# Kernel tuning notes

Hardware: AMD Instinct MI355X
Metric: run time of the kernel (lower is better)

Reference implementation:

```python
import jax, jax.numpy as jnp
import numpy as np

N, T0, T1 = 2, 4, 8
H, W = 128, 128
PD, AD = 4, 4
Z_POS, Z_APP = PD * PD, AD * AD
Z = Z_POS + Z_APP
KS, STRIDE, ROUTINGS = 3, 1, 3


def psquash(p, axis):
    return p / jnp.max(jnp.abs(p), axis=axis, keepdims=True)


def matwo_squash(p, axis):
    sq = jnp.sum(p * p, axis=axis, keepdims=True)
    return sq / (1.0 + sq) * p / jnp.sqrt(sq + 1e-9)


def setup_inputs() -> dict:
    key = jax.random.key(0)
    ks = jax.random.split(key, 5)
    return {
        "x": jax.random.normal(ks[0], (N, T0, Z, H, W), jnp.float32),
        "W_conv": jax.random.normal(ks[1], (T0, KS, KS, 1, T1), jnp.float32) * 0.1,
        "W_pos": jax.random.normal(ks[2], (T0, Z_POS, T1), jnp.float32) * 0.1,
        "W_app": jax.random.normal(ks[3], (T0, Z_APP, T1), jnp.float32) * 0.1,
        "b_app": jax.random.normal(ks[4], (T0, T1), jnp.float32) * 0.1,
    }


def _forward(x, W_conv, W_pos, W_app, b_app):
    n, t0, z0, h, w = x.shape
    t1 = W_conv.shape[-1]
    # per-input-capsule 2D conv: channels folded into batch, 1 -> t1 channels
    xt = x.transpose(1, 0, 2, 3, 4).reshape(t0, n * z0, h, w, 1)
    conv = jax.vmap(lambda u, k: jax.lax.conv_general_dilated(
        u, k, (STRIDE, STRIDE), 'SAME',
        dimension_numbers=('NHWC', 'HWIO', 'NHWC')))(xt, W_conv)
    h1, w1 = conv.shape[2], conv.shape[3]
    # [t0, N, z0, H1, W1, t1] -> [t0, N, H1, W1, t1, z0] -> flatten (t1,z0)
    u = conv.reshape(t0, n, z0, h1, w1, t1).transpose(0, 1, 3, 4, 5, 2)
    flat = u.reshape(t0, n, h1, w1, t1 * z0)
    # faithful replication of the original tf.split on the flattened (t1*z0) axis
    u_pos = flat[..., :t1 * Z_POS].reshape(t0, n, h1, w1, t1, PD, PD)
    u_app = flat[..., t1 * Z_POS:].reshape(t0, n, h1, w1, t1, AD, AD)

    # pose transform matrices: l2-normalize columns (axis=-2), coordinate addition
    mult_pos = W_pos.reshape(t0, t1, PD, PD)
    mult_pos = mult_pos / jnp.sqrt(
        jnp.maximum(jnp.sum(mult_pos * mult_pos, axis=-2, keepdims=True), 1e-12))
    coord = jnp.zeros((h1, w1, 1, PD, PD), x.dtype)
    coord = coord.at[:, :, 0, -1, 0].add(jnp.arange(w1, dtype=x.dtype)[None, :] / w1)
    coord = coord.at[:, :, 0, -1, 1].add(jnp.arange(h1, dtype=x.dtype)[:, None] / h1)
    mult_pos_hw = mult_pos[:, None, None] + coord[None]  # [t0,h1,w1,t1,PD,PD]
    u_hat_pos = jnp.einsum('cnhwtij,chwtjk->cnhwtik', u_pos, mult_pos_hw)

    mult_app = W_app.reshape(t0, t1, AD, AD)
    u_app = u_app + b_app[:, None, None, None, :, None, None]
    u_hat_app = jnp.einsum('cnhwtij,ctjk->cnhwtik', u_app, mult_app)

    u_hat = jnp.concatenate(
        [u_hat_pos.reshape(t0, n, h1, w1, t1, Z_POS),
         u_hat_app.reshape(t0, n, h1, w1, t1, Z_APP)], axis=-1)
    u_hat = u_hat.transpose(1, 5, 2, 3, 0, 4)  # [N, z1, H1, W1, t0, t1]

    # dual routing (sigmoid coupling, separate pos/app agreement)
    uh_pos, uh_app = u_hat[:, :Z_POS], u_hat[:, Z_POS:]
    b = jnp.zeros((n, h1, w1, t0, t1), x.dtype)
    for _ in range(ROUTINGS - 1):
        r = jax.nn.sigmoid(b)
        p = jnp.einsum('nzhwct,nhwct->nzhwt', u_hat, r)
        v_pos = psquash(p[:, :Z_POS], axis=1)
        v_app = matwo_squash(p[:, Z_POS:], axis=1)
        rout = (jnp.einsum('nzhwct,nzhwt->nhwct', uh_pos, v_pos)
                * jnp.einsum('nzhwct,nzhwt->nhwct', uh_app, v_app))
        b = b + rout
    c = jax.nn.sigmoid(b)
    p = jnp.einsum('nzhwct,nhwct->nzhwt', u_hat, c)
    v = jnp.concatenate([psquash(p[:, :Z_POS], axis=1),
                         matwo_squash(p[:, Z_POS:], axis=1)], axis=1)
    return v.transpose(0, 4, 1, 2, 3)  # [N, t1, z1, H1, W1]


def reference(x, W_conv, W_pos, W_app, b_app):
    return _forward(x, W_conv, W_pos, W_app, b_app)
```

## Files before the change

kernel.cpp:

```cpp
#include <hip/hip_runtime.h>
#include <cmath>


#define TH 2
#define TW 8
#define XR (TH + 2)
#define XC (TW + 2)
#define ZPAD 36

__device__ __forceinline__ float qsum4(float v) {
    int a = __builtin_amdgcn_mov_dpp(__float_as_int(v), 0xB1, 0xF, 0xF, true);
    v += __int_as_float(a);
    int b = __builtin_amdgcn_mov_dpp(__float_as_int(v), 0x4E, 0xF, 0xF, true);
    v += __int_as_float(b);
    return v;
}

__global__ __launch_bounds__(256)
__attribute__((amdgpu_waves_per_eu(4, 4)))
void caps_fused(const float* __restrict__ x,
                const float* __restrict__ Wc,
                const float* __restrict__ Wp,
                const float* __restrict__ Wa,
                const float* __restrict__ ba,
                float* __restrict__ out)
{
    __shared__ float xs[XR][XC][4][ZPAD];

    const int tid = threadIdx.x;
    const int n  = blockIdx.z;
    const int h0 = blockIdx.y * TH;
    const int w0 = blockIdx.x * TW;

    for (int e = tid; e < 128 * XR * XC; e += 256) {
        int col = e % XC;
        int tmp = e / XC;
        int row = tmp % XR;
        int cz  = tmp / XR;
        int gh = h0 - 1 + row;
        int gw = w0 - 1 + col;
        float v = 0.0f;
        if ((unsigned)gh < 128u && (unsigned)gw < 128u)
            v = x[(((size_t)(n * 128 + cz)) << 14) + (gh << 7) + gw];
        int z = cz & 31;
        int s = (row * XC + col) & 7;
        xs[row][col][cz >> 5][(((z >> 2) ^ s) << 2) | (z & 3)] = v;
    }

    const int p    = tid >> 5;
    const int lane = tid & 31;
    const int c    = lane & 3;
    const int t    = lane >> 2;
    const int chp  = t >> 1;
    const int q0   = (t & 1) << 2;

    float wp9[9], wa9[9];
#pragma unroll
    for (int i = 0; i < 9; ++i) {
        wp9[i] = Wc[(c * 9 + i) * 8 + chp];
        wa9[i] = Wc[(c * 9 + i) * 8 + 4 + chp];
    }
    float Mp[16], Ma[16];
#pragma unroll
    for (int q = 0; q < 16; ++q) {
        Mp[q] = Wp[c * 128 + t * 16 + q];
        Ma[q] = Wa[c * 128 + t * 16 + q];
    }
#pragma unroll
    for (int k = 0; k < 4; ++k) {
        float s = Mp[k] * Mp[k] + Mp[4 + k] * Mp[4 + k]
                + Mp[8 + k] * Mp[8 + k] + Mp[12 + k] * Mp[12 + k];
        float inv = __builtin_amdgcn_rsqf(fmaxf(s, 1e-12f));
        Mp[k] *= inv; Mp[4 + k] *= inv; Mp[8 + k] *= inv; Mp[12 + k] *= inv;
    }
    const float bap = ba[c * 8 + t];
    const float wx  = (float)(w0 + p) * (1.0f / 128.0f);

    __syncthreads();

    for (int g = 0; g < TH; ++g) {
        float up[16], ua[16];
#pragma unroll
        for (int q = 0; q < 16; ++q) { up[q] = 0.0f; ua[q] = 0.0f; }
#pragma unroll
        for (int dy = 0; dy < 3; ++dy) {
#pragma unroll
            for (int dx = 0; dx < 3; ++dx) {
                const int rr = g + dy, cc = p + dx;
                const int s = (rr * XC + cc) & 7;
                const float* bp = &xs[rr][cc][c][0];
                float xv[16];
                *(float4*)&xv[0]  = *(const float4*)(bp + (((q0 | 0) ^ s) << 2));
                *(float4*)&xv[4]  = *(const float4*)(bp + (((q0 | 1) ^ s) << 2));
                *(float4*)&xv[8]  = *(const float4*)(bp + (((q0 | 2) ^ s) << 2));
                *(float4*)&xv[12] = *(const float4*)(bp + (((q0 | 3) ^ s) << 2));
                const float w1 = wp9[dy * 3 + dx];
                const float w2 = wa9[dy * 3 + dx];
#pragma unroll
                for (int q = 0; q < 16; ++q) {
                    up[q] += xv[q] * w1;
                    ua[q] += xv[q] * w2;
                }
            }
        }

        const float hy = (float)(h0 + g) * (1.0f / 128.0f);
        float uh[32];
#pragma unroll
        for (int i = 0; i < 4; ++i) {
#pragma unroll
            for (int k = 0; k < 4; ++k) {
                uh[i * 4 + k] = up[i * 4 + 0] * Mp[k]
                              + up[i * 4 + 1] * Mp[4 + k]
                              + up[i * 4 + 2] * Mp[8 + k]
                              + up[i * 4 + 3] * Mp[12 + k];
            }
            uh[i * 4 + 0] += up[i * 4 + 3] * wx;
            uh[i * 4 + 1] += up[i * 4 + 3] * hy;
        }
#pragma unroll
        for (int i = 0; i < 4; ++i) {
            const float a0 = ua[i * 4 + 0] + bap;
            const float a1 = ua[i * 4 + 1] + bap;
            const float a2 = ua[i * 4 + 2] + bap;
            const float a3 = ua[i * 4 + 3] + bap;
#pragma unroll
            for (int k = 0; k < 4; ++k)
                uh[16 + i * 4 + k] = a0 * Ma[k] + a1 * Ma[4 + k]
                                   + a2 * Ma[8 + k] + a3 * Ma[12 + k];
        }

        float bacc = 0.0f;
#pragma unroll
        for (int it = 0; it < 3; ++it) {
            const float r = __builtin_amdgcn_rcpf(1.0f + __expf(-bacc));
            float pz[32];
#pragma unroll
            for (int zz = 0; zz < 32; ++zz)
                pz[zz] = qsum4(uh[zz] * r);

            float m01 = fmaxf(fabsf(pz[0]), fabsf(pz[1]));
            float m23 = fmaxf(fabsf(pz[2]), fabsf(pz[3]));
            float m45 = fmaxf(fabsf(pz[4]), fabsf(pz[5]));
            float m67 = fmaxf(fabsf(pz[6]), fabsf(pz[7]));
            float m89 = fmaxf(fabsf(pz[8]), fabsf(pz[9]));
            float mab = fmaxf(fabsf(pz[10]), fabsf(pz[11]));
            float mcd = fmaxf(fabsf(pz[12]), fabsf(pz[13]));
            float mef = fmaxf(fabsf(pz[14]), fabsf(pz[15]));
            float mx = fmaxf(fmaxf(fmaxf(m01, m23), fmaxf(m45, m67)),
                             fmaxf(fmaxf(m89, mab), fmaxf(mcd, mef)));
            const float invm = __builtin_amdgcn_rcpf(mx);
            float sq = 0.0f;
#pragma unroll
            for (int zz = 16; zz < 32; ++zz) sq += pz[zz] * pz[zz];
            const float fac = sq * __builtin_amdgcn_rcpf(1.0f + sq)
                                 * __builtin_amdgcn_rsqf(sq + 1e-9f);

            if (it < 2) {
                float dp = 0.0f, da = 0.0f;
#pragma unroll
                for (int zz = 0; zz < 16; ++zz) dp += uh[zz] * pz[zz];
#pragma unroll
                for (int zz = 16; zz < 32; ++zz) da += uh[zz] * pz[zz];
                bacc += (dp * invm) * (da * fac);
            } else if (c == 0) {
                const int row = h0 + g;
                float* ob = out + (((size_t)((n * 8 + t) * 32)) << 14)
                                + (row << 7) + (w0 + p);
#pragma unroll
                for (int zz = 0; zz < 16; ++zz)
                    ob[((size_t)zz) << 14] = pz[zz] * invm;
#pragma unroll
                for (int zz = 16; zz < 32; ++zz)
                    ob[((size_t)zz) << 14] = pz[zz] * fac;
            }
        }
    }
}

extern "C" void kernel_launch(void* const* d_in, const int* in_sizes, int n_in,
                              void* d_out, int out_size, void* d_ws, size_t ws_size,
                              hipStream_t stream) {
    const float* x  = (const float*)d_in[0];
    const float* Wc = (const float*)d_in[1];
    const float* Wp = (const float*)d_in[2];
    const float* Wa = (const float*)d_in[3];
    const float* ba = (const float*)d_in[4];
    float* out = (float*)d_out;

    dim3 grid(128 / TW, 128 / TH, 2);
    caps_fused<<<grid, 256, 0, stream>>>(x, Wc, Wp, Wa, ba, out);
}
```

Baseline: 133.0 us.

## Enlarge row tile, restructure halo load, and specialize first routing iteration

Result: faster. 121.5 us (-8.7%).

```diff
diff --git a/kernel.cpp b/kernel.cpp
--- a/kernel.cpp
+++ b/kernel.cpp
@@ -2,11 +2,10 @@
 #include <cmath>
 
 
-#define TH 2
+#define TH 4
 #define TW 8
 #define XR (TH + 2)
 #define XC (TW + 2)
-#define ZPAD 36
 
 __device__ __forceinline__ float qsum4(float v) {
     int a = __builtin_amdgcn_mov_dpp(__float_as_int(v), 0xB1, 0xF, 0xF, true);
@@ -16,8 +15,7 @@
     return v;
 }
 
-__global__ __launch_bounds__(256)
-__attribute__((amdgpu_waves_per_eu(4, 4)))
+__global__ __launch_bounds__(256, 4)
 void caps_fused(const float* __restrict__ x,
                 const float* __restrict__ Wc,
                 const float* __restrict__ Wp,
@@ -25,26 +23,32 @@
                 const float* __restrict__ ba,
                 float* __restrict__ out)
 {
-    __shared__ float xs[XR][XC][4][ZPAD];
+    __shared__ float xs[XR][XC][4][36];
 
     const int tid = threadIdx.x;
     const int n  = blockIdx.z;
     const int h0 = blockIdx.y * TH;
     const int w0 = blockIdx.x * TW;
 
-    for (int e = tid; e < 128 * XR * XC; e += 256) {
-        int col = e % XC;
-        int tmp = e / XC;
-        int row = tmp % XR;
-        int cz  = tmp / XR;
-        int gh = h0 - 1 + row;
-        int gw = w0 - 1 + col;
-        float v = 0.0f;
-        if ((unsigned)gh < 128u && (unsigned)gw < 128u)
-            v = x[(((size_t)(n * 128 + cz)) << 14) + (gh << 7) + gw];
-        int z = cz & 31;
-        int s = (row * XC + col) & 7;
-        xs[row][col][cz >> 5][(((z >> 2) ^ s) << 2) | (z & 3)] = v;
+    {
+        const int rc = tid & 63;
+        const int tq = tid >> 6;
+        if (rc < 60) {
+            const int row = rc / 10;
+            const int col = rc - row * 10;
+            const int gh = h0 - 1 + row;
+            const int gw = w0 - 1 + col;
+            const bool valid = ((unsigned)gh < 128u) & ((unsigned)gw < 128u);
+            const int s = rc & 7;
+            float* lb = &xs[0][0][0][0] + rc * 144 + tq;
+            const float* gp = x + (((size_t)(n * 128 + tq)) << 14)
+                                + (gh << 7) + gw;
+#pragma unroll
+            for (int k = 0; k < 32; ++k) {
+                float v = valid ? gp[((size_t)(4 * k)) << 14] : 0.0f;
+                lb[(k >> 3) * 36 + (((k & 7) ^ s) << 2)] = v;
+            }
+        }
     }
 
     const int p    = tid >> 5;
@@ -78,6 +82,7 @@
 
     __syncthreads();
 
+#pragma unroll 1
     for (int g = 0; g < TH; ++g) {
         float up[16], ua[16];
 #pragma unroll
@@ -130,9 +135,36 @@
                                    + a2 * Ma[8 + k] + a3 * Ma[12 + k];
         }
 
-        float bacc = 0.0f;
-#pragma unroll
-        for (int it = 0; it < 3; ++it) {
+        float bacc;
+        {
+            float S[32];
+#pragma unroll
+            for (int zz = 0; zz < 32; ++zz) S[zz] = qsum4(uh[zz]);
+            float m01 = fmaxf(fabsf(S[0]), fabsf(S[1]));
+            float m23 = fmaxf(fabsf(S[2]), fabsf(S[3]));
+            float m45 = fmaxf(fabsf(S[4]), fabsf(S[5]));
+            float m67 = fmaxf(fabsf(S[6]), fabsf(S[7]));
+            float m89 = fmaxf(fabsf(S[8]), fabsf(S[9]));
+            float mab = fmaxf(fabsf(S[10]), fabsf(S[11]));
+            float mcd = fmaxf(fabsf(S[12]), fabsf(S[13]));
+            float mef = fmaxf(fabsf(S[14]), fabsf(S[15]));
+            const float mxS = fmaxf(fmaxf(fmaxf(m01, m23), fmaxf(m45, m67)),
+                                    fmaxf(fmaxf(m89, mab), fmaxf(mcd, mef)));
+            float dpS = 0.0f, daS = 0.0f, sqS = 0.0f;
+#pragma unroll
+            for (int zz = 0; zz < 16; ++zz) dpS += uh[zz] * S[zz];
+#pragma unroll
+            for (int zz = 16; zz < 32; ++zz) {
+                sqS += S[zz] * S[zz];
+                daS += uh[zz] * S[zz];
+            }
+            const float sq = 0.25f * sqS;
+            const float fac = sq * __builtin_amdgcn_rcpf(1.0f + sq)
+                                 * __builtin_amdgcn_rsqf(sq + 1e-9f);
+            bacc = (dpS * __builtin_amdgcn_rcpf(mxS)) * (0.5f * daS * fac);
+        }
+#pragma unroll
+        for (int it = 1; it < 3; ++it) {
             const float r = __builtin_amdgcn_rcpf(1.0f + __expf(-bacc));
             float pz[32];
 #pragma unroll
@@ -147,8 +179,8 @@
             float mab = fmaxf(fabsf(pz[10]), fabsf(pz[11]));
             float mcd = fmaxf(fabsf(pz[12]), fabsf(pz[13]));
             float mef = fmaxf(fabsf(pz[14]), fabsf(pz[15]));
-            float mx = fmaxf(fmaxf(fmaxf(m01, m23), fmaxf(m45, m67)),
-                             fmaxf(fmaxf(m89, mab), fmaxf(mcd, mef)));
+            const float mx = fmaxf(fmaxf(fmaxf(m01, m23), fmaxf(m45, m67)),
+                                   fmaxf(fmaxf(m89, mab), fmaxf(mcd, mef)));
             const float invm = __builtin_amdgcn_rcpf(mx);
             float sq = 0.0f;
 #pragma unroll
```
